# Kernel optimization log

Measured on AMD Instinct MI355X. Metric: run time of the kernel, lower is better.

Reference implementation:

```python
import jax, jax.numpy as jnp
import numpy as np

B, L, C, K = 8, 16384, 64, 7
NORM_FACTOR = 1.0
LN_EPS = 1e-6


def setup_inputs() -> dict:
    key = jax.random.key(0)
    k0, k1, k2 = jax.random.split(key, 3)
    x = jax.random.normal(k0, (B, L, C), dtype=jnp.float32)
    # lecun_normal-style init for (C_out, C_in, K) dynamic-conv weights
    weights = jax.random.normal(k1, (C, C, K), dtype=jnp.float32) / np.float32(np.sqrt(C))
    ln_scale = jnp.ones((C,), dtype=jnp.float32)
    ln_bias = jnp.zeros((C,), dtype=jnp.float32)
    conv_kernel = jax.random.normal(k2, (C, C), dtype=jnp.float32) / np.float32(np.sqrt(C))
    conv_bias = jnp.zeros((C,), dtype=jnp.float32)
    prelu_slope = jnp.asarray(0.01, dtype=jnp.float32)
    return {"x": x, "weights": weights, "ln_scale": ln_scale, "ln_bias": ln_bias,
            "conv_kernel": conv_kernel, "conv_bias": conv_bias, "prelu_slope": prelu_slope}


def reference(x, weights, ln_scale, ln_bias, conv_kernel, conv_bias, prelu_slope):
    b, l, c = x.shape
    k = weights.shape[-1]
    x0 = x  # residual source, (B, L, C)

    # im2col unfold over sequence: window 2K, stride 2, no padding
    p = jax.lax.conv_general_dilated_patches(
        jnp.transpose(x, (0, 2, 1)),  # (B, C, L)
        filter_shape=(2 * k,), window_strides=(2,), padding=((0, 0),))
    t = p.shape[-1]  # out_len = (L - 2K)//2 + 1
    p = jnp.reshape(p, (b, c, 2 * k, t))
    p = jnp.transpose(p, (0, 1, 3, 2))  # (B, C, T, 2K)

    # dynamic weights from the trailing 2T inputs: (B, 2T, C) x (C, C, K) -> (B, C, 2T, K)
    w = jnp.einsum('blc,dck->bdlk', x0[:, -(t * 2):, :], weights)
    even_seq = w[:, :, ::2, :]   # (B, C, T, K)
    odd_seq = w[:, :, 1::2, :]   # (B, C, T, K)
    w = jnp.stack([even_seq, odd_seq], axis=-1)         # (B, C, T, K, 2)
    w = jnp.reshape(w, (b, c, t, k * 2))                # interleaved (B, C, T, 2K)
    w = jnp.tanh(w / NORM_FACTOR)

    # gated windowed sum
    y = jnp.sum(p * w, axis=3)          # (B, C, T)
    y = jnp.transpose(y, (0, 2, 1))     # (B, T, C)

    # inner skip: stride-2 subsample of input, aligned to the tail
    y = x0[:, ::2, :][:, -t:, :] + y

    # LayerNorm over channel dim (flax default eps=1e-6, with scale and bias)
    mu = jnp.mean(y, axis=-1, keepdims=True)
    var = jnp.mean(jnp.square(y - mu), axis=-1, keepdims=True)
    yn = (y - mu) * jax.lax.rsqrt(var + LN_EPS) * ln_scale + ln_bias

    # 1x1 conv + PReLU + outer skip
    z = jnp.einsum('btc,co->bto', yn, conv_kernel) + conv_bias
    z = jnp.where(z >= 0, z, prelu_slope * z)
    return yn + z
```

## Files before the change

### kernel.cpp

```cpp
#include <hip/hip_runtime.h>
#include <stdint.h>

#define BB 8
#define LLEN 16384
#define CC 64
#define TOUT 8186
#define TILE_T 32
#define NROWS 76
#define SXS 68
#define SXGS 72
#define YNS 66
#define YNBS 76

typedef __attribute__((ext_vector_type(8))) short short8;
typedef __attribute__((ext_vector_type(4))) float float4v;
typedef __attribute__((ext_vector_type(4))) unsigned short ushort4v;

__device__ inline unsigned short f2bf(float f) {
  union { float f; uint32_t u; } v; v.f = f;
  uint32_t r = v.u + 0x7fffu + ((v.u >> 16) & 1u);
  return (unsigned short)(r >> 16);
}
__device__ inline float rcp_fast(float x) {
  float r; asm("v_rcp_f32 %0, %1" : "=v"(r) : "v"(x)); return r;
}
__device__ inline float tanh_fast(float a) {
  float t = fminf(fmaxf(a, -3.4f), 3.4f);
  float s = t * t;
  float u = 105.0f + s;
  float v = 945.0f + s * u;
  float w = __builtin_fmaf(s, 15.0f, 420.0f);
  float d = __builtin_fmaf(s, w, 945.0f);
  return (t * v) * rcp_fast(d);
}

__global__ void prep_frags(const float* __restrict__ weights,
                           const float* __restrict__ ck,
                           unsigned short* __restrict__ wfrag,
                           unsigned short* __restrict__ ckfrag)
{
  int bid = blockIdx.x, tid = threadIdx.x;
  if (bid < 56) {
    int nt = bid >> 1, kh = bid & 1;
    for (int e = tid; e < 512; e += 256) {
      int ln = e >> 3, j = e & 7;
      int kk = nt >> 2;
      int d  = (nt & 3) * 16 + (ln & 15);
      int cp = kh * 32 + (ln >> 4) * 8 + j;
      wfrag[(bid * 64 + ln) * 8 + j] = f2bf(weights[d * 448 + cp * 7 + kk]);
    }
  } else {
    int bb2 = bid - 56;
    int nt = bb2 >> 1, kh = bb2 & 1;
    for (int e = tid; e < 512; e += 256) {
      int ln = e >> 3, j = e & 7;
      int oo = nt * 16 + (ln & 15);
      int c2 = kh * 32 + (ln >> 4) * 8 + j;
      ckfrag[(bb2 * 64 + ln) * 8 + j] = f2bf(ck[c2 * 64 + oo]);
    }
  }
}

__global__ __launch_bounds__(256, 4)
void convblock_main(const float* __restrict__ x,
                    const unsigned short* __restrict__ wfrag,
                    const unsigned short* __restrict__ ckfrag,
                    const float* __restrict__ ln_scale,
                    const float* __restrict__ ln_bias,
                    const float* __restrict__ conv_bias,
                    const float* __restrict__ prelu_slope,
                    float* __restrict__ out)
{
  __shared__ __align__(16) char smem[29888];
  float*          sx2 = (float*)smem;
  unsigned short* ynb = (unsigned short*)smem;
  unsigned short* sxg = (unsigned short*)(smem + 20672);
  float*          ynf = (float*)(smem + 20672);

  const int tid  = threadIdx.x;
  const int b    = blockIdx.x >> 8;
  const int t0   = (blockIdx.x & 255) * TILE_T;
  const int lane = tid & 63;
  const int w    = tid >> 6;
  const int l15  = tid & 15;
  const int q    = (tid >> 4) & 3;

  {
    const float* xb = x + (size_t)b * ((size_t)LLEN * CC);
    #pragma unroll
    for (int i = 0; i < 5; ++i) {
      int idx = tid + i * 256;
      if (idx < NROWS * 16) {
        int row = idx >> 4, f4 = idx & 15, c0 = f4 * 4;
        int rowg = 2 * t0 + row;
        if (rowg > LLEN - 1) rowg = LLEN - 1;
        float4v v = *(const float4v*)(xb + (size_t)rowg * CC + c0);
        int base = row * SXS + 16 * (f4 & 3) + (f4 >> 2);
        sx2[base + 0]  = v[0];
        sx2[base + 4]  = v[1];
        sx2[base + 8]  = v[2];
        sx2[base + 12] = v[3];
        if (row >= 12) {
          ushort4v p;
          p[0] = f2bf(v[0]); p[1] = f2bf(v[1]); p[2] = f2bf(v[2]); p[3] = f2bf(v[3]);
          *(ushort4v*)&sxg[(row - 12) * SXGS + c0] = p;
        }
      }
    }
  }
  float lnS[4], lnB[4];
  #pragma unroll
  for (int dq = 0; dq < 4; ++dq) {
    lnS[dq] = ln_scale[16 * dq + l15];
    lnB[dq] = ln_bias[16 * dq + l15];
  }
  __syncthreads();

  short8 a0 = *(const short8*)&sxg[(16 * w + l15) * SXGS + q * 8];
  short8 a1 = *(const short8*)&sxg[(16 * w + l15) * SXGS + 32 + q * 8];
  __syncthreads();

  float y[2][4];
  #pragma unroll
  for (int dlt = 0; dlt < 2; ++dlt)
    #pragma unroll
    for (int dq = 0; dq < 4; ++dq) y[dlt][dq] = 0.f;

  const float4v zacc = (float4v){0.f, 0.f, 0.f, 0.f};
  const int dtbase = 8 * w + 2 * q;
  #pragma unroll
  for (int kk = 0; kk < 7; ++kk) {
    float4v acc[4];
    #pragma unroll
    for (int dq = 0; dq < 4; ++dq) {
      int nt = kk * 4 + dq;
      short8 b0 = *(const short8*)&wfrag[((nt * 2 + 0) * 64 + lane) * 8];
      short8 b1 = *(const short8*)&wfrag[((nt * 2 + 1) * 64 + lane) * 8];
      float4v a = __builtin_amdgcn_mfma_f32_16x16x32_bf16(a0, b0, zacc, 0, 0, 0);
      a = __builtin_amdgcn_mfma_f32_16x16x32_bf16(a1, b1, a, 0, 0, 0);
      acc[dq] = a;
    }
    #pragma unroll
    for (int dlt = 0; dlt < 2; ++dlt) {
      int rowe = 2 * (dtbase + dlt) + 2 * kk;
      float4v xe = *(const float4v*)&sx2[rowe * SXS + l15 * 4];
      float4v xo = *(const float4v*)&sx2[(rowe + 1) * SXS + l15 * 4];
      #pragma unroll
      for (int dq = 0; dq < 4; ++dq) {
        float ge = tanh_fast(acc[dq][2 * dlt + 0]);
        float go = tanh_fast(acc[dq][2 * dlt + 1]);
        y[dlt][dq] += xe[dq] * ge + xo[dq] * go;
        if (kk == 6) y[dlt][dq] += xe[dq];
      }
    }
  }

  float ynr[2][4];
  #pragma unroll
  for (int dlt = 0; dlt < 2; ++dlt) {
    float s1 = y[dlt][0] + y[dlt][1] + y[dlt][2] + y[dlt][3];
    float s2 = y[dlt][0]*y[dlt][0] + y[dlt][1]*y[dlt][1]
             + y[dlt][2]*y[dlt][2] + y[dlt][3]*y[dlt][3];
    #pragma unroll
    for (int m = 1; m < 16; m <<= 1) {
      s1 += __shfl_xor(s1, m, 64);
      s2 += __shfl_xor(s2, m, 64);
    }
    float mu   = s1 * (1.0f / 64.0f);
    float var  = s2 * (1.0f / 64.0f) - mu * mu;
    float rstd = rsqrtf(var + 1e-6f);
    int dt = dtbase + dlt;
    #pragma unroll
    for (int dq = 0; dq < 4; ++dq) {
      float yn = (y[dlt][dq] - mu) * rstd * lnS[dq] + lnB[dq];
      ynr[dlt][dq] = yn;
      ynf[dt * YNS + 16 * dq + l15] = yn;
    }
  }
  __syncthreads();

  #pragma unroll
  for (int dlt = 0; dlt < 2; ++dlt)
    #pragma unroll
    for (int dq = 0; dq < 4; ++dq)
      ynb[(dtbase + dlt) * YNBS + 16 * dq + l15] = f2bf(ynr[dlt][dq]);
  __syncthreads();

  const float sl = prelu_slope[0];
  const int   o  = 16 * w + l15;
  const float cb = conv_bias[o];
  short8 bf0 = *(const short8*)&ckfrag[((w * 2 + 0) * 64 + lane) * 8];
  short8 bf1 = *(const short8*)&ckfrag[((w * 2 + 1) * 64 + lane) * 8];
  #pragma unroll
  for (int mt = 0; mt < 2; ++mt) {
    short8 af0 = *(const short8*)&ynb[(mt * 16 + l15) * YNBS + q * 8];
    short8 af1 = *(const short8*)&ynb[(mt * 16 + l15) * YNBS + 32 + q * 8];
    float4v zc = __builtin_amdgcn_mfma_f32_16x16x32_bf16(af0, bf0, zacc, 0, 0, 0);
    zc = __builtin_amdgcn_mfma_f32_16x16x32_bf16(af1, bf1, zc, 0, 0, 0);
    #pragma unroll
    for (int r = 0; r < 4; ++r) {
      int t  = mt * 16 + 4 * q + r;
      int tg = t0 + t;
      if (tg < TOUT) {
        float z = zc[r] + cb;
        z = (z >= 0.f) ? z : sl * z;
        out[((size_t)b * TOUT + tg) * CC + o] = ynf[t * YNS + o] + z;
      }
    }
  }
}

extern "C" void kernel_launch(void* const* d_in, const int* in_sizes, int n_in,
                              void* d_out, int out_size, void* d_ws, size_t ws_size,
                              hipStream_t stream)
{
  const float* x        = (const float*)d_in[0];
  const float* weights  = (const float*)d_in[1];
  const float* ln_scale = (const float*)d_in[2];
  const float* ln_bias  = (const float*)d_in[3];
  const float* ck       = (const float*)d_in[4];
  const float* cb       = (const float*)d_in[5];
  const float* slope    = (const float*)d_in[6];
  unsigned short* wfrag  = (unsigned short*)d_ws;
  unsigned short* ckfrag = (unsigned short*)((char*)d_ws + 57344);

  prep_frags<<<64, 256, 0, stream>>>(weights, ck, wfrag, ckfrag);
  convblock_main<<<BB * 256, 256, 0, stream>>>(x, wfrag, ckfrag, ln_scale,
                                               ln_bias, cb, slope, (float*)d_out);
}
```

Measured before the change: 118.8 us.

## Store x tile as packed bf16 even/odd pairs in swizzled LDS

The staged input tile now holds bf16 instead of fp32, with each even/odd row pair packed into one 32-bit word and an XOR swizzle on the channel index to avoid bank conflicts. This roughly halves LDS use, so launch bounds rise to 6 blocks per SM for more occupancy. The windowed sum needs one 16-byte LDS load per step instead of two. The cost is lower precision in the gated sum and in the residual term taken from x.

```diff
diff --git a/kernel.cpp b/kernel.cpp
--- a/kernel.cpp
+++ b/kernel.cpp
@@ -6,14 +6,15 @@
 #define CC 64
 #define TOUT 8186
 #define TILE_T 32
-#define NROWS 76
-#define SXS 68
+#define NPAIR 38
+#define SXPS 68
 #define SXGS 72
 #define YNS 66
 #define YNBS 76
 
 typedef __attribute__((ext_vector_type(8))) short short8;
 typedef __attribute__((ext_vector_type(4))) float float4v;
+typedef __attribute__((ext_vector_type(4))) unsigned int uint4v;
 typedef __attribute__((ext_vector_type(4))) unsigned short ushort4v;
 
 __device__ inline unsigned short f2bf(float f) {
@@ -61,7 +62,7 @@
   }
 }
 
-__global__ __launch_bounds__(256, 4)
+__global__ __launch_bounds__(256, 6)
 void convblock_main(const float* __restrict__ x,
                     const unsigned short* __restrict__ wfrag,
                     const unsigned short* __restrict__ ckfrag,
@@ -71,11 +72,11 @@
                     const float* __restrict__ prelu_slope,
                     float* __restrict__ out)
 {
-  __shared__ __align__(16) char smem[29888];
-  float*          sx2 = (float*)smem;
+  __shared__ __align__(16) char smem[19552];
+  uint32_t*       sxp = (uint32_t*)smem;
   unsigned short* ynb = (unsigned short*)smem;
-  unsigned short* sxg = (unsigned short*)(smem + 20672);
-  float*          ynf = (float*)(smem + 20672);
+  unsigned short* sxg = (unsigned short*)(smem + 10336);
+  float*          ynf = (float*)(smem + 10336);
 
   const int tid  = threadIdx.x;
   const int b    = blockIdx.x >> 8;
@@ -88,23 +89,28 @@
   {
     const float* xb = x + (size_t)b * ((size_t)LLEN * CC);
     #pragma unroll
-    for (int i = 0; i < 5; ++i) {
-      int idx = tid + i * 256;
-      if (idx < NROWS * 16) {
-        int row = idx >> 4, f4 = idx & 15, c0 = f4 * 4;
-        int rowg = 2 * t0 + row;
-        if (rowg > LLEN - 1) rowg = LLEN - 1;
-        float4v v = *(const float4v*)(xb + (size_t)rowg * CC + c0);
-        int base = row * SXS + 16 * (f4 & 3) + (f4 >> 2);
-        sx2[base + 0]  = v[0];
-        sx2[base + 4]  = v[1];
-        sx2[base + 8]  = v[2];
-        sx2[base + 12] = v[3];
-        if (row >= 12) {
-          ushort4v p;
-          p[0] = f2bf(v[0]); p[1] = f2bf(v[1]); p[2] = f2bf(v[2]); p[3] = f2bf(v[3]);
-          *(ushort4v*)&sxg[(row - 12) * SXGS + c0] = p;
+    for (int i = 0; i < 3; ++i) {
+      int u = tid + i * 256;
+      if (u < NPAIR * 16) {
+        int rp = u >> 4, f4 = u & 15, c0 = f4 * 4;
+        int g0 = 2 * t0 + 2 * rp, g1 = g0 + 1;
+        if (g0 > LLEN - 1) g0 = LLEN - 1;
+        if (g1 > LLEN - 1) g1 = LLEN - 1;
+        float4v ve = *(const float4v*)(xb + (size_t)g0 * CC + c0);
+        float4v vo = *(const float4v*)(xb + (size_t)g1 * CC + c0);
+        ushort4v pe, po;
+        #pragma unroll
+        for (int j = 0; j < 4; ++j) { pe[j] = f2bf(ve[j]); po[j] = f2bf(vo[j]); }
+        int sw = rp & 7;
+        #pragma unroll
+        for (int j = 0; j < 4; ++j) {
+          int c = c0 + j;
+          sxp[rp * SXPS + (((c & 15) ^ sw) << 2) + (c >> 4)] =
+              (uint32_t)pe[j] | ((uint32_t)po[j] << 16);
         }
+        int r0 = 2 * rp, r1 = r0 + 1;
+        if (r0 >= 12) *(ushort4v*)&sxg[(r0 - 12) * SXGS + c0] = pe;
+        if (r1 >= 12) *(ushort4v*)&sxg[(r1 - 12) * SXGS + c0] = po;
       }
     }
   }
@@ -142,15 +148,17 @@
     }
     #pragma unroll
     for (int dlt = 0; dlt < 2; ++dlt) {
-      int rowe = 2 * (dtbase + dlt) + 2 * kk;
-      float4v xe = *(const float4v*)&sx2[rowe * SXS + l15 * 4];
-      float4v xo = *(const float4v*)&sx2[(rowe + 1) * SXS + l15 * 4];
+      int rp = dtbase + dlt + kk;
+      uint4v pr = *(const uint4v*)&sxp[rp * SXPS + ((l15 ^ (rp & 7)) << 2)];
       #pragma unroll
       for (int dq = 0; dq < 4; ++dq) {
+        uint32_t u = pr[dq];
+        float xe = __uint_as_float(u << 16);
+        float xo = __uint_as_float(u & 0xffff0000u);
         float ge = tanh_fast(acc[dq][2 * dlt + 0]);
         float go = tanh_fast(acc[dq][2 * dlt + 1]);
-        y[dlt][dq] += xe[dq] * ge + xo[dq] * go;
-        if (kk == 6) y[dlt][dq] += xe[dq];
+        y[dlt][dq] += xe * ge + xo * go;
+        if (kk == 6) y[dlt][dq] += xe;
       }
     }
   }
```

Measured after the change: 243.7 us. 105% more time.
